# Optimization experiments

Hardware: AMD Instinct MI355X
Metric: run time of the kernel (lower is better)

The kernel has to match this reference:

```python
import jax, jax.numpy as jnp
import numpy as np

PICK_WIN = 20      # int(round(pick_win_s / dt)) = int(round(2.0 / 0.1))
W_PICK = 0.1
BETA = 25.0


def setup_inputs() -> dict:
    key = jax.random.key(0)
    k1, k2 = jax.random.split(key)
    B, T = 4096, 6000
    pred = jax.random.normal(k1, (B, T), dtype=jnp.float32)
    target = jax.random.normal(k2, (B, T), dtype=jnp.float32)
    return {"pred": pred, "target": target}


def _windowed_soft_argmax(x, mask, pos):
    # soft_argmax(|x[s:e]|, beta) + s  ==  sum_j softmax(beta*|x_j| over j in [s,e)) * j
    logits = jnp.where(mask, BETA * jnp.abs(x), -jnp.inf)  # [B, T]
    p = jax.nn.softmax(logits, axis=-1)
    return jnp.sum(p * pos.astype(x.dtype), axis=-1)       # [B]


def reference(pred, target):
    loss = jnp.mean(jnp.abs(pred - target))  # nn.L1Loss (mean)

    T = target.shape[-1]
    center = jnp.argmax(jnp.abs(target), axis=-1)          # [B]
    pos = jnp.arange(T)                                     # [T]
    # window [max(0, c-W), min(T, c+W)) expressed as a mask over absolute positions
    mask = (pos[None, :] >= center[:, None] - PICK_WIN) & (pos[None, :] < center[:, None] + PICK_WIN)

    picks_pred = _windowed_soft_argmax(pred, mask, pos)
    picks_true = _windowed_soft_argmax(target, mask, pos)

    pick_loss = jnp.mean(jnp.abs(picks_pred - picks_true)) / T
    return loss + W_PICK * pick_loss
```

## Files before the change

### kernel.cpp

```cpp
#include <hip/hip_runtime.h>
#include <math.h>
#include <limits.h>
#include <stdint.h>

#define T_LEN 6000
#define B_ROWS 4096
#define PICK_WIN 20
#define BETA 25.0f

typedef float f4 __attribute__((ext_vector_type(4)));

__global__ __launch_bounds__(256) void row_pass1(const float* __restrict__ pred,
                                                 const float* __restrict__ target,
                                                 float* __restrict__ row_l1,
                                                 float* __restrict__ row_pick) {
    const int row  = blockIdx.x;
    const int tid  = threadIdx.x;
    const int wave = tid >> 6;
    const int lane = tid & 63;

    const uint64_t pb = (uint64_t)(pred   + (size_t)row * T_LEN);
    const uint64_t tb = (uint64_t)(target + (size_t)row * T_LEN);

    const bool has6 = (tid < (T_LEN / 4 - 5 * 256));
    const uint32_t v0 = (uint32_t)tid * 16u;
    const uint32_t v1 = v0 + 1u * 4096u;
    const uint32_t v2 = v0 + 2u * 4096u;
    const uint32_t v3 = v0 + 3u * 4096u;
    const uint32_t v4 = v0 + 4u * 4096u;
    const uint32_t v5 = has6 ? (v0 + 5u * 4096u) : (uint32_t)((T_LEN / 4 - 1) * 16);

    f4 p0, p1, p2, p3, p4, p5, t0, t1, t2, t3, t4, t5;
    asm volatile(
        "global_load_dwordx4 %0,  %12, %18\n\t"
        "global_load_dwordx4 %1,  %13, %18\n\t"
        "global_load_dwordx4 %2,  %14, %18\n\t"
        "global_load_dwordx4 %3,  %15, %18\n\t"
        "global_load_dwordx4 %4,  %16, %18\n\t"
        "global_load_dwordx4 %5,  %17, %18\n\t"
        "global_load_dwordx4 %6,  %12, %19\n\t"
        "global_load_dwordx4 %7,  %13, %19\n\t"
        "global_load_dwordx4 %8,  %14, %19\n\t"
        "global_load_dwordx4 %9,  %15, %19\n\t"
        "global_load_dwordx4 %10, %16, %19\n\t"
        "global_load_dwordx4 %11, %17, %19\n\t"
        "s_waitcnt vmcnt(0)"
        : "=&v"(p0), "=&v"(p1), "=&v"(p2), "=&v"(p3), "=&v"(p4), "=&v"(p5),
          "=&v"(t0), "=&v"(t1), "=&v"(t2), "=&v"(t3), "=&v"(t4), "=&v"(t5)
        : "v"(v0), "v"(v1), "v"(v2), "v"(v3), "v"(v4), "v"(v5),
          "s"(pb), "s"(tb));
    __builtin_amdgcn_sched_barrier(0);

    float sum   = 0.0f;
    float bestv = -1.0f;
    int   besti = INT_MAX;

#define CONSUME(PP, TT, K)                                                     \
    do {                                                                       \
        const int base = (tid + (K) * 256) * 4;                                \
        sum += fabsf(PP.x - TT.x) + fabsf(PP.y - TT.y) +                       \
               fabsf(PP.z - TT.z) + fabsf(PP.w - TT.w);                        \
        float a_;                                                              \
        a_ = fabsf(TT.x); if (a_ > bestv) { bestv = a_; besti = base;     }    \
        a_ = fabsf(TT.y); if (a_ > bestv) { bestv = a_; besti = base + 1; }    \
        a_ = fabsf(TT.z); if (a_ > bestv) { bestv = a_; besti = base + 2; }    \
        a_ = fabsf(TT.w); if (a_ > bestv) { bestv = a_; besti = base + 3; }    \
    } while (0)

    CONSUME(p0, t0, 0);
    CONSUME(p1, t1, 1);
    CONSUME(p2, t2, 2);
    CONSUME(p3, t3, 3);
    CONSUME(p4, t4, 4);
    if (has6) CONSUME(p5, t5, 5);
#undef CONSUME

    #pragma unroll
    for (int o = 32; o > 0; o >>= 1) {
        sum += __shfl_xor(sum, o);
        const float ov = __shfl_xor(bestv, o);
        const int   oi = __shfl_xor(besti, o);
        if (ov > bestv || (ov == bestv && oi < besti)) { bestv = ov; besti = oi; }
    }

    __shared__ float s_sum[4];
    __shared__ float s_val[4];
    __shared__ int   s_idx[4];
    if (lane == 0) { s_sum[wave] = sum; s_val[wave] = bestv; s_idx[wave] = besti; }
    __syncthreads();

    if (tid < 64) {
        float bs = 0.0f, bv = -1.0f;
        int   bi = INT_MAX;
        #pragma unroll
        for (int w = 0; w < 4; ++w) {
            bs += s_sum[w];
            if (s_val[w] > bv || (s_val[w] == bv && s_idx[w] < bi)) {
                bv = s_val[w]; bi = s_idx[w];
            }
        }

        const int c   = bi;
        const int s   = max(0, c - PICK_WIN);
        const int e   = min(T_LEN, c + PICK_WIN);
        const int len = e - s;

        float ap = -INFINITY, at = -INFINITY;
        const float posf = (float)(s + tid);
        if (tid < len) {
            const size_t idx = (size_t)row * T_LEN + s + tid;
            ap = BETA * fabsf(pred[idx]);
            at = BETA * fabsf(target[idx]);
        }

        float mp = ap, mt = at;
        #pragma unroll
        for (int o = 32; o > 0; o >>= 1) {
            mp = fmaxf(mp, __shfl_xor(mp, o));
            mt = fmaxf(mt, __shfl_xor(mt, o));
        }

        float wp = 0.0f, wt = 0.0f, wpp = 0.0f, wtp = 0.0f;
        if (tid < len) {
            wp  = expf(ap - mp);
            wt  = expf(at - mt);
            wpp = wp * posf;
            wtp = wt * posf;
        }
        #pragma unroll
        for (int o = 32; o > 0; o >>= 1) {
            wp  += __shfl_xor(wp,  o);
            wt  += __shfl_xor(wt,  o);
            wpp += __shfl_xor(wpp, o);
            wtp += __shfl_xor(wtp, o);
        }

        if (tid == 0) {
            row_l1[row]   = bs;
            row_pick[row] = fabsf(wpp / wp - wtp / wt);
        }
    }
}

__global__ __launch_bounds__(256) void finalize(const float* __restrict__ row_l1,
                                                const float* __restrict__ row_pick,
                                                float* __restrict__ out) {
    const int tid  = threadIdx.x;
    const int wave = tid >> 6;
    const int lane = tid & 63;
    float a = 0.0f, b = 0.0f;
    for (int i = tid; i < B_ROWS; i += 256) {
        a += row_l1[i];
        b += row_pick[i];
    }
    #pragma unroll
    for (int o = 32; o > 0; o >>= 1) {
        a += __shfl_xor(a, o);
        b += __shfl_xor(b, o);
    }
    __shared__ float f1[4], f2[4];
    if (lane == 0) { f1[wave] = a; f2[wave] = b; }
    __syncthreads();
    if (tid == 0) {
        const float ta = f1[0] + f1[1] + f1[2] + f1[3];
        const float tb = f2[0] + f2[1] + f2[2] + f2[3];
        const float loss = ta / (float)((long long)B_ROWS * (long long)T_LEN);
        const float pick = (tb / (float)B_ROWS) / (float)T_LEN;
        out[0] = loss + 0.1f * pick;
    }
}

extern "C" void kernel_launch(void* const* d_in, const int* in_sizes, int n_in,
                              void* d_out, int out_size, void* d_ws, size_t ws_size,
                              hipStream_t stream) {
    const float* pred   = (const float*)d_in[0];
    const float* target = (const float*)d_in[1];
    float* out = (float*)d_out;

    float* row_l1   = (float*)d_ws;
    float* row_pick = row_l1 + B_ROWS;

    row_pass1<<<B_ROWS, 256, 0, stream>>>(pred, target, row_l1, row_pick);
    finalize<<<1, 256, 0, stream>>>(row_l1, row_pick, out);
}
```

Measured before the change: 40.42 us.

## Process two rows per block with staged loads and vectorize finalize reduction

Each block now handles two rows. It issues all loads for both rows up front and consumes the first row after a partial vmcnt wait, so its compute overlaps the second row's loads. The window soft-argmax for the two rows runs in parallel on two separate waves. Finalize switches to unrolled float4 loads. The cost is doubled register pressure (48 vector registers of loaded data per thread), which may lower occupancy, and half as many blocks.

```diff
diff --git a/kernel.cpp b/kernel.cpp
--- a/kernel.cpp
+++ b/kernel.cpp
@@ -14,13 +14,16 @@
                                                  const float* __restrict__ target,
                                                  float* __restrict__ row_l1,
                                                  float* __restrict__ row_pick) {
-    const int row  = blockIdx.x;
+    const int row0 = blockIdx.x * 2;
+    const int row1 = row0 + 1;
     const int tid  = threadIdx.x;
     const int wave = tid >> 6;
     const int lane = tid & 63;
 
-    const uint64_t pb = (uint64_t)(pred   + (size_t)row * T_LEN);
-    const uint64_t tb = (uint64_t)(target + (size_t)row * T_LEN);
+    const uint64_t pb0 = (uint64_t)(pred   + (size_t)row0 * T_LEN);
+    const uint64_t tb0 = (uint64_t)(target + (size_t)row0 * T_LEN);
+    const uint64_t pb1 = (uint64_t)(pred   + (size_t)row1 * T_LEN);
+    const uint64_t tb1 = (uint64_t)(target + (size_t)row1 * T_LEN);
 
     const bool has6 = (tid < (T_LEN / 4 - 5 * 256));
     const uint32_t v0 = (uint32_t)tid * 16u;
@@ -30,7 +33,8 @@
     const uint32_t v4 = v0 + 4u * 4096u;
     const uint32_t v5 = has6 ? (v0 + 5u * 4096u) : (uint32_t)((T_LEN / 4 - 1) * 16);
 
-    f4 p0, p1, p2, p3, p4, p5, t0, t1, t2, t3, t4, t5;
+    f4 a0, a1, a2, a3, a4, a5, b0, b1, b2, b3, b4, b5;
+    f4 c0, c1, c2, c3, c4, c5, d0, d1, d2, d3, d4, d5;
     asm volatile(
         "global_load_dwordx4 %0,  %12, %18\n\t"
         "global_load_dwordx4 %1,  %13, %18\n\t"
@@ -43,60 +47,95 @@
         "global_load_dwordx4 %8,  %14, %19\n\t"
         "global_load_dwordx4 %9,  %15, %19\n\t"
         "global_load_dwordx4 %10, %16, %19\n\t"
-        "global_load_dwordx4 %11, %17, %19\n\t"
-        "s_waitcnt vmcnt(0)"
-        : "=&v"(p0), "=&v"(p1), "=&v"(p2), "=&v"(p3), "=&v"(p4), "=&v"(p5),
-          "=&v"(t0), "=&v"(t1), "=&v"(t2), "=&v"(t3), "=&v"(t4), "=&v"(t5)
+        "global_load_dwordx4 %11, %17, %19"
+        : "=&v"(a0), "=&v"(a1), "=&v"(a2), "=&v"(a3), "=&v"(a4), "=&v"(a5),
+          "=&v"(b0), "=&v"(b1), "=&v"(b2), "=&v"(b3), "=&v"(b4), "=&v"(b5)
         : "v"(v0), "v"(v1), "v"(v2), "v"(v3), "v"(v4), "v"(v5),
-          "s"(pb), "s"(tb));
-    __builtin_amdgcn_sched_barrier(0);
-
-    float sum   = 0.0f;
-    float bestv = -1.0f;
-    int   besti = INT_MAX;
-
-#define CONSUME(PP, TT, K)                                                     \
+          "s"(pb0), "s"(tb0));
+    asm volatile(
+        "global_load_dwordx4 %0,  %12, %18\n\t"
+        "global_load_dwordx4 %1,  %13, %18\n\t"
+        "global_load_dwordx4 %2,  %14, %18\n\t"
+        "global_load_dwordx4 %3,  %15, %18\n\t"
+        "global_load_dwordx4 %4,  %16, %18\n\t"
+        "global_load_dwordx4 %5,  %17, %18\n\t"
+        "global_load_dwordx4 %6,  %12, %19\n\t"
+        "global_load_dwordx4 %7,  %13, %19\n\t"
+        "global_load_dwordx4 %8,  %14, %19\n\t"
+        "global_load_dwordx4 %9,  %15, %19\n\t"
+        "global_load_dwordx4 %10, %16, %19\n\t"
+        "global_load_dwordx4 %11, %17, %19"
+        : "=&v"(c0), "=&v"(c1), "=&v"(c2), "=&v"(c3), "=&v"(c4), "=&v"(c5),
+          "=&v"(d0), "=&v"(d1), "=&v"(d2), "=&v"(d3), "=&v"(d4), "=&v"(d5)
+        : "v"(v0), "v"(v1), "v"(v2), "v"(v3), "v"(v4), "v"(v5),
+          "s"(pb1), "s"(tb1));
+
+    float sum0 = 0.0f, sum1 = 0.0f;
+    float bv0 = -1.0f, bv1 = -1.0f;
+    int   bi0 = INT_MAX, bi1 = INT_MAX;
+
+#define CONSUME(PP, TT, K, SUM, BV, BI)                                        \
     do {                                                                       \
         const int base = (tid + (K) * 256) * 4;                                \
-        sum += fabsf(PP.x - TT.x) + fabsf(PP.y - TT.y) +                       \
+        SUM += fabsf(PP.x - TT.x) + fabsf(PP.y - TT.y) +                       \
                fabsf(PP.z - TT.z) + fabsf(PP.w - TT.w);                        \
         float a_;                                                              \
-        a_ = fabsf(TT.x); if (a_ > bestv) { bestv = a_; besti = base;     }    \
-        a_ = fabsf(TT.y); if (a_ > bestv) { bestv = a_; besti = base + 1; }    \
-        a_ = fabsf(TT.z); if (a_ > bestv) { bestv = a_; besti = base + 2; }    \
-        a_ = fabsf(TT.w); if (a_ > bestv) { bestv = a_; besti = base + 3; }    \
+        a_ = fabsf(TT.x); if (a_ > BV) { BV = a_; BI = base;     }             \
+        a_ = fabsf(TT.y); if (a_ > BV) { BV = a_; BI = base + 1; }             \
+        a_ = fabsf(TT.z); if (a_ > BV) { BV = a_; BI = base + 2; }             \
+        a_ = fabsf(TT.w); if (a_ > BV) { BV = a_; BI = base + 3; }             \
     } while (0)
 
-    CONSUME(p0, t0, 0);
-    CONSUME(p1, t1, 1);
-    CONSUME(p2, t2, 2);
-    CONSUME(p3, t3, 3);
-    CONSUME(p4, t4, 4);
-    if (has6) CONSUME(p5, t5, 5);
+    asm volatile("s_waitcnt vmcnt(12)" ::: "memory");
+    __builtin_amdgcn_sched_barrier(0);
+    CONSUME(a0, b0, 0, sum0, bv0, bi0);
+    CONSUME(a1, b1, 1, sum0, bv0, bi0);
+    CONSUME(a2, b2, 2, sum0, bv0, bi0);
+    CONSUME(a3, b3, 3, sum0, bv0, bi0);
+    CONSUME(a4, b4, 4, sum0, bv0, bi0);
+    if (has6) CONSUME(a5, b5, 5, sum0, bv0, bi0);
+
+    asm volatile("s_waitcnt vmcnt(0)" ::: "memory");
+    __builtin_amdgcn_sched_barrier(0);
+    CONSUME(c0, d0, 0, sum1, bv1, bi1);
+    CONSUME(c1, d1, 1, sum1, bv1, bi1);
+    CONSUME(c2, d2, 2, sum1, bv1, bi1);
+    CONSUME(c3, d3, 3, sum1, bv1, bi1);
+    CONSUME(c4, d4, 4, sum1, bv1, bi1);
+    if (has6) CONSUME(c5, d5, 5, sum1, bv1, bi1);
 #undef CONSUME
 
     #pragma unroll
     for (int o = 32; o > 0; o >>= 1) {
-        sum += __shfl_xor(sum, o);
-        const float ov = __shfl_xor(bestv, o);
-        const int   oi = __shfl_xor(besti, o);
-        if (ov > bestv || (ov == bestv && oi < besti)) { bestv = ov; besti = oi; }
-    }
-
-    __shared__ float s_sum[4];
-    __shared__ float s_val[4];
-    __shared__ int   s_idx[4];
-    if (lane == 0) { s_sum[wave] = sum; s_val[wave] = bestv; s_idx[wave] = besti; }
+        sum0 += __shfl_xor(sum0, o);
+        sum1 += __shfl_xor(sum1, o);
+        const float ov0 = __shfl_xor(bv0, o);
+        const int   oi0 = __shfl_xor(bi0, o);
+        const float ov1 = __shfl_xor(bv1, o);
+        const int   oi1 = __shfl_xor(bi1, o);
+        if (ov0 > bv0 || (ov0 == bv0 && oi0 < bi0)) { bv0 = ov0; bi0 = oi0; }
+        if (ov1 > bv1 || (ov1 == bv1 && oi1 < bi1)) { bv1 = ov1; bi1 = oi1; }
+    }
+
+    __shared__ float s_sum[2][4];
+    __shared__ float s_val[2][4];
+    __shared__ int   s_idx[2][4];
+    if (lane == 0) {
+        s_sum[0][wave] = sum0; s_val[0][wave] = bv0; s_idx[0][wave] = bi0;
+        s_sum[1][wave] = sum1; s_val[1][wave] = bv1; s_idx[1][wave] = bi1;
+    }
     __syncthreads();
 
-    if (tid < 64) {
+    if (wave < 2) {
+        const int r = wave;
+        const int row = row0 + r;
         float bs = 0.0f, bv = -1.0f;
         int   bi = INT_MAX;
         #pragma unroll
         for (int w = 0; w < 4; ++w) {
-            bs += s_sum[w];
-            if (s_val[w] > bv || (s_val[w] == bv && s_idx[w] < bi)) {
-                bv = s_val[w]; bi = s_idx[w];
+            bs += s_sum[r][w];
+            if (s_val[r][w] > bv || (s_val[r][w] == bv && s_idx[r][w] < bi)) {
+                bv = s_val[r][w]; bi = s_idx[r][w];
             }
         }
 
@@ -106,9 +145,9 @@
         const int len = e - s;
 
         float ap = -INFINITY, at = -INFINITY;
-        const float posf = (float)(s + tid);
-        if (tid < len) {
-            const size_t idx = (size_t)row * T_LEN + s + tid;
+        const float posf = (float)(s + lane);
+        if (lane < len) {
+            const size_t idx = (size_t)row * T_LEN + s + lane;
             ap = BETA * fabsf(pred[idx]);
             at = BETA * fabsf(target[idx]);
         }
@@ -121,7 +160,7 @@
         }
 
         float wp = 0.0f, wt = 0.0f, wpp = 0.0f, wtp = 0.0f;
-        if (tid < len) {
+        if (lane < len) {
             wp  = expf(ap - mp);
             wt  = expf(at - mt);
             wpp = wp * posf;
@@ -135,7 +174,7 @@
             wtp += __shfl_xor(wtp, o);
         }
 
-        if (tid == 0) {
+        if (lane == 0) {
             row_l1[row]   = bs;
             row_pick[row] = fabsf(wpp / wp - wtp / wt);
         }
@@ -148,10 +187,16 @@
     const int tid  = threadIdx.x;
     const int wave = tid >> 6;
     const int lane = tid & 63;
+    const f4* l4 = (const f4*)row_l1;
+    const f4* p4 = (const f4*)row_pick;
+
     float a = 0.0f, b = 0.0f;
-    for (int i = tid; i < B_ROWS; i += 256) {
-        a += row_l1[i];
-        b += row_pick[i];
+    #pragma unroll
+    for (int k = 0; k < 4; ++k) {
+        const f4 x = l4[tid + k * 256];
+        const f4 y = p4[tid + k * 256];
+        a += x.x + x.y + x.z + x.w;
+        b += y.x + y.y + y.z + y.w;
     }
     #pragma unroll
     for (int o = 32; o > 0; o >>= 1) {
@@ -180,6 +225,6 @@
     float* row_l1   = (float*)d_ws;
     float* row_pick = row_l1 + B_ROWS;
 
-    row_pass1<<<B_ROWS, 256, 0, stream>>>(pred, target, row_l1, row_pick);
+    row_pass1<<<B_ROWS / 2, 256, 0, stream>>>(pred, target, row_l1, row_pick);
     finalize<<<1, 256, 0, stream>>>(row_l1, row_pick, out);
 }
```

After: 37.48 us, median of 2. -7.3%, faster.

## Halve row block size, double per-thread loads, and split waitcnt to overlap consume

Applied to the files above, without the earlier changes.

Each row is now handled by 128 threads instead of 256, so every thread issues 24 vector loads in two interleaved asm batches. A partial s_waitcnt vmcnt(12) lets the first half of the data be consumed while the second half is still arriving. The cross-wave reduction shrinks to two waves, and the finalize kernel reads with float4 vector loads. The goal is more memory-level parallelism per thread and less reduction and sync overhead, at the cost of higher VGPR pressure that may lower occupancy.

```diff
diff --git a/kernel.cpp b/kernel.cpp
--- a/kernel.cpp
+++ b/kernel.cpp
@@ -10,7 +10,7 @@
 
 typedef float f4 __attribute__((ext_vector_type(4)));
 
-__global__ __launch_bounds__(256) void row_pass1(const float* __restrict__ pred,
+__global__ __launch_bounds__(128) void row_pass1(const float* __restrict__ pred,
                                                  const float* __restrict__ target,
                                                  float* __restrict__ row_l1,
                                                  float* __restrict__ row_pick) {
@@ -22,34 +22,50 @@
     const uint64_t pb = (uint64_t)(pred   + (size_t)row * T_LEN);
     const uint64_t tb = (uint64_t)(target + (size_t)row * T_LEN);
 
-    const bool has6 = (tid < (T_LEN / 4 - 5 * 256));
-    const uint32_t v0 = (uint32_t)tid * 16u;
-    const uint32_t v1 = v0 + 1u * 4096u;
-    const uint32_t v2 = v0 + 2u * 4096u;
-    const uint32_t v3 = v0 + 3u * 4096u;
-    const uint32_t v4 = v0 + 4u * 4096u;
-    const uint32_t v5 = has6 ? (v0 + 5u * 4096u) : (uint32_t)((T_LEN / 4 - 1) * 16);
-
-    f4 p0, p1, p2, p3, p4, p5, t0, t1, t2, t3, t4, t5;
+    const bool has12 = (tid < (T_LEN / 4 - 11 * 128));
+    uint32_t va[12];
+    #pragma unroll
+    for (int k = 0; k < 11; ++k) va[k] = (uint32_t)(tid + k * 128) * 16u;
+    va[11] = has12 ? (uint32_t)(tid + 11 * 128) * 16u
+                   : (uint32_t)((T_LEN / 4 - 1) * 16);
+
+    f4 p0, p1, p2, p3, p4, p5, p6, p7, p8, p9, p10, p11;
+    f4 t0, t1, t2, t3, t4, t5, t6, t7, t8, t9, t10, t11;
+
     asm volatile(
         "global_load_dwordx4 %0,  %12, %18\n\t"
+        "global_load_dwordx4 %6,  %12, %19\n\t"
         "global_load_dwordx4 %1,  %13, %18\n\t"
+        "global_load_dwordx4 %7,  %13, %19\n\t"
         "global_load_dwordx4 %2,  %14, %18\n\t"
+        "global_load_dwordx4 %8,  %14, %19\n\t"
         "global_load_dwordx4 %3,  %15, %18\n\t"
+        "global_load_dwordx4 %9,  %15, %19\n\t"
         "global_load_dwordx4 %4,  %16, %18\n\t"
+        "global_load_dwordx4 %10, %16, %19\n\t"
         "global_load_dwordx4 %5,  %17, %18\n\t"
-        "global_load_dwordx4 %6,  %12, %19\n\t"
-        "global_load_dwordx4 %7,  %13, %19\n\t"
-        "global_load_dwordx4 %8,  %14, %19\n\t"
-        "global_load_dwordx4 %9,  %15, %19\n\t"
-        "global_load_dwordx4 %10, %16, %19\n\t"
-        "global_load_dwordx4 %11, %17, %19\n\t"
-        "s_waitcnt vmcnt(0)"
+        "global_load_dwordx4 %11, %17, %19"
         : "=&v"(p0), "=&v"(p1), "=&v"(p2), "=&v"(p3), "=&v"(p4), "=&v"(p5),
           "=&v"(t0), "=&v"(t1), "=&v"(t2), "=&v"(t3), "=&v"(t4), "=&v"(t5)
-        : "v"(v0), "v"(v1), "v"(v2), "v"(v3), "v"(v4), "v"(v5),
+        : "v"(va[0]), "v"(va[1]), "v"(va[2]), "v"(va[3]), "v"(va[4]), "v"(va[5]),
           "s"(pb), "s"(tb));
-    __builtin_amdgcn_sched_barrier(0);
+    asm volatile(
+        "global_load_dwordx4 %0,  %12, %18\n\t"
+        "global_load_dwordx4 %6,  %12, %19\n\t"
+        "global_load_dwordx4 %1,  %13, %18\n\t"
+        "global_load_dwordx4 %7,  %13, %19\n\t"
+        "global_load_dwordx4 %2,  %14, %18\n\t"
+        "global_load_dwordx4 %8,  %14, %19\n\t"
+        "global_load_dwordx4 %3,  %15, %18\n\t"
+        "global_load_dwordx4 %9,  %15, %19\n\t"
+        "global_load_dwordx4 %4,  %16, %18\n\t"
+        "global_load_dwordx4 %10, %16, %19\n\t"
+        "global_load_dwordx4 %5,  %17, %18\n\t"
+        "global_load_dwordx4 %11, %17, %19"
+        : "=&v"(p6), "=&v"(p7), "=&v"(p8), "=&v"(p9), "=&v"(p10), "=&v"(p11),
+          "=&v"(t6), "=&v"(t7), "=&v"(t8), "=&v"(t9), "=&v"(t10), "=&v"(t11)
+        : "v"(va[6]), "v"(va[7]), "v"(va[8]), "v"(va[9]), "v"(va[10]), "v"(va[11]),
+          "s"(pb), "s"(tb));
 
     float sum   = 0.0f;
     float bestv = -1.0f;
@@ -57,7 +73,7 @@
 
 #define CONSUME(PP, TT, K)                                                     \
     do {                                                                       \
-        const int base = (tid + (K) * 256) * 4;                                \
+        const int base = (tid + (K) * 128) * 4;                                \
         sum += fabsf(PP.x - TT.x) + fabsf(PP.y - TT.y) +                       \
                fabsf(PP.z - TT.z) + fabsf(PP.w - TT.w);                        \
         float a_;                                                              \
@@ -67,12 +83,23 @@
         a_ = fabsf(TT.w); if (a_ > bestv) { bestv = a_; besti = base + 3; }    \
     } while (0)
 
+    asm volatile("s_waitcnt vmcnt(12)" ::: "memory");
+    __builtin_amdgcn_sched_barrier(0);
     CONSUME(p0, t0, 0);
     CONSUME(p1, t1, 1);
     CONSUME(p2, t2, 2);
     CONSUME(p3, t3, 3);
     CONSUME(p4, t4, 4);
-    if (has6) CONSUME(p5, t5, 5);
+    CONSUME(p5, t5, 5);
+
+    asm volatile("s_waitcnt vmcnt(0)" ::: "memory");
+    __builtin_amdgcn_sched_barrier(0);
+    CONSUME(p6,  t6,  6);
+    CONSUME(p7,  t7,  7);
+    CONSUME(p8,  t8,  8);
+    CONSUME(p9,  t9,  9);
+    CONSUME(p10, t10, 10);
+    if (has12) CONSUME(p11, t11, 11);
 #undef CONSUME
 
     #pragma unroll
@@ -83,21 +110,18 @@
         if (ov > bestv || (ov == bestv && oi < besti)) { bestv = ov; besti = oi; }
     }
 
-    __shared__ float s_sum[4];
-    __shared__ float s_val[4];
-    __shared__ int   s_idx[4];
+    __shared__ float s_sum[2];
+    __shared__ float s_val[2];
+    __shared__ int   s_idx[2];
     if (lane == 0) { s_sum[wave] = sum; s_val[wave] = bestv; s_idx[wave] = besti; }
     __syncthreads();
 
     if (tid < 64) {
-        float bs = 0.0f, bv = -1.0f;
-        int   bi = INT_MAX;
-        #pragma unroll
-        for (int w = 0; w < 4; ++w) {
-            bs += s_sum[w];
-            if (s_val[w] > bv || (s_val[w] == bv && s_idx[w] < bi)) {
-                bv = s_val[w]; bi = s_idx[w];
-            }
+        float bs = s_sum[0] + s_sum[1];
+        float bv = s_val[0];
+        int   bi = s_idx[0];
+        if (s_val[1] > bv || (s_val[1] == bv && s_idx[1] < bi)) {
+            bv = s_val[1]; bi = s_idx[1];
         }
 
         const int c   = bi;
@@ -148,10 +172,16 @@
     const int tid  = threadIdx.x;
     const int wave = tid >> 6;
     const int lane = tid & 63;
+    const f4* l4 = (const f4*)row_l1;
+    const f4* p4 = (const f4*)row_pick;
+
     float a = 0.0f, b = 0.0f;
-    for (int i = tid; i < B_ROWS; i += 256) {
-        a += row_l1[i];
-        b += row_pick[i];
+    #pragma unroll
+    for (int k = 0; k < 4; ++k) {
+        const f4 x = l4[tid + k * 256];
+        const f4 y = p4[tid + k * 256];
+        a += x.x + x.y + x.z + x.w;
+        b += y.x + y.y + y.z + y.w;
     }
     #pragma unroll
     for (int o = 32; o > 0; o >>= 1) {
@@ -180,6 +210,6 @@
     float* row_l1   = (float*)d_ws;
     float* row_pick = row_l1 + B_ROWS;
 
-    row_pass1<<<B_ROWS, 256, 0, stream>>>(pred, target, row_l1, row_pick);
+    row_pass1<<<B_ROWS, 128, 0, stream>>>(pred, target, row_l1, row_pick);
     finalize<<<1, 256, 0, stream>>>(row_l1, row_pick, out);
 }
```

Result: faster. 37.84 us (-6.4%).
